# Kernel optimization log

Hardware: AMD Instinct MI355X
Metric: run time of the kernel (lower is better)

The kernel has to match this reference:

```python
import jax, jax.numpy as jnp
import numpy as np

H = 2048          # hidden_size
NH = 16           # num_attention_heads
HD = H // NH      # head_dim = 128
RD = HD // 2      # rotary dim = 64
LAT = H // 8      # latent_dim = 256
B, S = 2, 2048
BASE = 10000.0


def rotary_emb(seq_len, dtype=jnp.float32):
    # DeepseekRotaryEmbedding(dim=RD): inv_freq over arange(0, RD, 2)
    inv_freq = 1.0 / (BASE ** (np.arange(0, RD, 2, dtype=np.float32) / RD))  # [RD//2]
    pos = jnp.arange(seq_len, dtype=dtype)
    sincos = pos[:, None] * jnp.asarray(inv_freq, dtype)                     # [S, RD//2]
    return jnp.concatenate([jnp.sin(sincos), jnp.cos(sincos)], axis=-1)      # [S, RD]


def apply_rope(x, emb):
    # x: [B, S, NH, RD]; emb: [S, RD] with sin first half, cos second half
    half = RD // 2
    x1, x2 = x[..., :half], x[..., half:]
    sin = emb[:, None, :half]   # [S, 1, half] broadcast over heads
    cos = emb[:, None, half:]
    return jnp.concatenate([x1 * cos - x2 * sin, x1 * sin + x2 * cos], axis=-1)


def setup_inputs() -> dict:
    key = jax.random.key(0)
    ks = jax.random.split(key, 9)
    def w(k, shape):
        return jax.random.normal(k, shape, dtype=jnp.float32) * (1.0 / np.sqrt(shape[-1]))
    return {
        "hidden_states": jax.random.normal(ks[0], (B, S, H), dtype=jnp.float32),
        "W_kv_d": w(ks[1], (LAT, H)),
        "W_q_d": w(ks[2], (LAT, H)),
        "W_k_u": w(ks[3], (H // 2, LAT)),
        "W_q_u": w(ks[4], (H // 2, LAT)),
        "W_v_u": w(ks[5], (H, LAT)),
        "W_rope_k": w(ks[6], (H // 2, H)),
        "W_rope_q": w(ks[7], (H // 2, LAT)),
        "W_o": w(ks[8], (H, H)),
    }


def reference(hidden_states, W_kv_d, W_q_d, W_k_u, W_q_u, W_v_u, W_rope_k, W_rope_q, W_o):
    x = hidden_states                                   # [B, S, H]
    kv_d = x @ W_kv_d.T                                 # [B, S, LAT]
    q_d = x @ W_q_d.T                                   # [B, S, LAT]
    k_c = (kv_d @ W_k_u.T).reshape(B, S, NH, RD)        # content half of k
    q_c = (q_d @ W_q_u.T).reshape(B, S, NH, RD)
    v = (kv_d @ W_v_u.T).reshape(B, S, NH, HD)
    k_r = (x @ W_rope_k.T).reshape(B, S, NH, RD)
    q_r = (q_d @ W_rope_q.T).reshape(B, S, NH, RD)

    emb = rotary_emb(S, x.dtype)                        # [S, RD]
    q_r = apply_rope(q_r, emb)
    k_r = apply_rope(k_r, emb)

    q = jnp.concatenate([q_c, q_r], axis=-1)            # [B, S, NH, HD]
    k = jnp.concatenate([k_c, k_r], axis=-1)

    scale = 1.0 / np.sqrt(HD)                           # SDPA default scale
    scores = jnp.einsum("bqhd,bkhd->bhqk", q, k) * scale
    causal = jnp.tril(jnp.ones((S, S), dtype=bool))
    scores = jnp.where(causal, scores, jnp.finfo(scores.dtype).min)
    probs = jax.nn.softmax(scores, axis=-1)
    y = jnp.einsum("bhqk,bkhd->bqhd", probs, v).reshape(B, S, H)
    return y @ W_o.T
```

## Files before the change

kernel.cpp:

```cpp
#include <hip/hip_runtime.h>

typedef unsigned short u16;
typedef unsigned int u32;
typedef __attribute__((ext_vector_type(8))) short bf16x8;
typedef __attribute__((ext_vector_type(4))) float f32x4;

#define DEVI static __device__ __forceinline__

DEVI u16 f2b(float f){
  u32 x = __float_as_uint(f);
  return (u16)((x + 0x7fffu + ((x >> 16) & 1u)) >> 16);
}
DEVI float b2f(u16 u){ return __uint_as_float(((u32)u) << 16); }
DEVI float2 up2(u32 u){
  return make_float2(__uint_as_float(u << 16), __uint_as_float(u & 0xffff0000u));
}
DEVI u32 pk2(float a, float b){
  u32 ua = __float_as_uint(a) + 0x8000u;
  u32 ub = __float_as_uint(b) + 0x8000u;
  return (ua >> 16) | (ub & 0xffff0000u);
}
DEVI void gload16(const u16* g, u16* l){
  __builtin_amdgcn_global_load_lds((const __attribute__((address_space(1))) void*)g,
                                   (__attribute__((address_space(3))) void*)l,
                                   16, 0, 0);
}

#define QSCALE 0.12751744900929456f

struct CSrc { const float* s[9]; };
__global__ void cvt_all(CSrc cs, u16* __restrict__ xb, u16* __restrict__ wcat){
  int i = blockIdx.x * 256 + threadIdx.x;
  if (i >= 4259840) return;
  const float4* s; int lo, di; uint2* d;
  if (i < 2097152){
    s = (const float4*)cs.s[0]; lo = 0; di = i; d = (uint2*)xb;
  } else {
    int j = i - 2097152; di = j; d = (uint2*)wcat;
    if      (j <  131072){ s = (const float4*)cs.s[1]; lo = 0;       }
    else if (j <  262144){ s = (const float4*)cs.s[2]; lo = 131072;  }
    else if (j <  786432){ s = (const float4*)cs.s[3]; lo = 262144;  }
    else if (j <  851968){ s = (const float4*)cs.s[4]; lo = 786432;  }
    else if (j <  917504){ s = (const float4*)cs.s[5]; lo = 851968;  }
    else if (j <  983040){ s = (const float4*)cs.s[6]; lo = 917504;  }
    else if (j < 1114112){ s = (const float4*)cs.s[7]; lo = 983040;  }
    else                 { s = (const float4*)cs.s[8]; lo = 1114112; }
  }
  float4 f = s[di - lo];
  u32 a = (u32)f2b(f.x) | ((u32)f2b(f.y) << 16);
  u32 b = (u32)f2b(f.z) | ((u32)f2b(f.w) << 16);
  d[di] = make_uint2(a, b);
}

template<int MODE>
__global__ __launch_bounds__(256, 2)
void gemm_bt(const u16* __restrict__ A, int lda, const u16* __restrict__ W,
             void* __restrict__ D, int N, int K){
  __shared__ u16 As[128 * 64];
  __shared__ u16 Bs[128 * 64];
  const int tid = threadIdx.x;
  const int wave = tid >> 6, lane = tid & 63;
  const int lr = lane & 15, lk = lane >> 4;
  int bid = blockIdx.y * gridDim.x + blockIdx.x;
  const int nwg = gridDim.x * gridDim.y;
  bid = (bid & 7) * (nwg >> 3) + (bid >> 3);
  const int bx = bid % gridDim.x, by = bid / gridDim.x;
  const int m0 = by * 128, n0 = bx * 128;
  const int wm = wave >> 1, wn = wave & 1;
  f32x4 acc[4][4] = {};

  const int srow = tid >> 3;
  const int scol = ((tid & 7) ^ (srow & 7)) << 3;
  const u16* ag = A + (size_t)(m0 + srow) * lda + scol;
  const u16* bg = W + (size_t)(n0 + srow) * K + scol;
  u16* lA = As + wave * 512;
  u16* lB = Bs + wave * 512;

  for (int k0 = 0; k0 < K; k0 += 64){
    __syncthreads();
    #pragma unroll
    for (int s = 0; s < 4; ++s){
      gload16(ag + (size_t)s * 32 * lda + k0, lA + s * 2048);
      gload16(bg + (size_t)s * 32 * K   + k0, lB + s * 2048);
    }
    asm volatile("s_waitcnt vmcnt(0)" ::: "memory");
    __syncthreads();
    #pragma unroll
    for (int ks = 0; ks < 2; ++ks){
      bf16x8 af[4], bfr[4];
      const int perm = ((ks * 4 + lk) ^ (lr & 7)) << 3;
      #pragma unroll
      for (int i = 0; i < 4; i++)
        af[i] = *(const bf16x8*)(As + (wm * 64 + i * 16 + lr) * 64 + perm);
      #pragma unroll
      for (int j = 0; j < 4; j++)
        bfr[j] = *(const bf16x8*)(Bs + (wn * 64 + j * 16 + lr) * 64 + perm);
      #pragma unroll
      for (int i = 0; i < 4; i++)
        #pragma unroll
        for (int j = 0; j < 4; j++)
          acc[i][j] = __builtin_amdgcn_mfma_f32_16x16x32_bf16(af[i], bfr[j], acc[i][j], 0, 0, 0);
    }
  }

  const int rb = (lane >> 4) * 4, cl = lane & 15;
  #pragma unroll
  for (int i = 0; i < 4; i++){
    #pragma unroll
    for (int j = 0; j < 4; j++){
      const int mb = m0 + wm * 64 + i * 16 + rb;
      const int n  = n0 + wn * 64 + j * 16 + cl;
      #pragma unroll
      for (int r = 0; r < 4; r++){
        int m = mb + r;
        float v = acc[i][j][r];
        if (MODE == 0) ((u16*)D)[(size_t)m * N + n] = f2b(v);
        else           ((float*)D)[(size_t)m * N + n] = v;
      }
    }
  }
}

__global__ __launch_bounds__(256, 2)
void gemm_up(const u16* __restrict__ dcat, const u16* __restrict__ qW,
             const u16* __restrict__ kvW, u16* __restrict__ qbuf,
             u16* __restrict__ qrp, u16* __restrict__ kbuf, u16* __restrict__ vt){
  __shared__ u16 As[128 * 32];
  __shared__ u16 Bs[128 * 32];
  const int tid = threadIdx.x;
  const int wave = tid >> 6, lane = tid & 63;
  const int lr = lane & 15, lk = lane >> 4;
  int bid = blockIdx.y * 40 + blockIdx.x;
  bid = (bid & 7) * 160 + (bid >> 3);
  const int bx = bid % 40, by = bid / 40;
  const bool qside = bx < 16;
  const u16* A = qside ? dcat + 256 : dcat;
  const u16* W = qside ? qW : kvW;
  const int n0 = (qside ? bx : bx - 16) * 128;
  const int m0 = by * 128;
  const int wm = wave >> 1, wn = wave & 1;
  f32x4 acc[4][4] = {};

  const u16* a0 = A + (size_t)(m0 + (tid >> 2)) * 1536 + (tid & 3) * 8;
  const u16* a1 = a0 + (size_t)64 * 1536;
  const u16* b0 = W + (size_t)(n0 + (tid >> 2)) * 256 + (tid & 3) * 8;
  const u16* b1 = b0 + (size_t)64 * 256;
  u16* lA0 = As + wave * 512;  u16* lA1 = As + 2048 + wave * 512;
  u16* lB0 = Bs + wave * 512;  u16* lB1 = Bs + 2048 + wave * 512;

  for (int k0 = 0; k0 < 256; k0 += 32){
    __syncthreads();
    gload16(a0 + k0, lA0);
    gload16(a1 + k0, lA1);
    gload16(b0 + k0, lB0);
    gload16(b1 + k0, lB1);
    asm volatile("s_waitcnt vmcnt(0)" ::: "memory");
    __syncthreads();
    bf16x8 af[4], bfr[4];
    #pragma unroll
    for (int i = 0; i < 4; i++)
      af[i] = *(const bf16x8*)(As + (wm * 64 + i * 16 + lr) * 32 + lk * 8);
    #pragma unroll
    for (int j = 0; j < 4; j++)
      bfr[j] = *(const bf16x8*)(Bs + (wn * 64 + j * 16 + lr) * 32 + lk * 8);
    #pragma unroll
    for (int i = 0; i < 4; i++)
      #pragma unroll
      for (int j = 0; j < 4; j++)
        acc[i][j] = __builtin_amdgcn_mfma_f32_16x16x32_bf16(af[i], bfr[j], acc[i][j], 0, 0, 0);
  }

  const int rb = (lane >> 4) * 4, cl = lane & 15;
  #pragma unroll
  for (int i = 0; i < 4; i++){
    #pragma unroll
    for (int j = 0; j < 4; j++){
      const int mb = m0 + wm * 64 + i * 16 + rb;
      const int n  = n0 + wn * 64 + j * 16 + cl;
      if (!qside && n >= 1024){
        int n1 = n - 1024, h = n1 >> 7, d = n1 & 127, b = mb >> 11, s = mb & 2047;
        u32 lo = (u32)f2b(acc[i][j][0]) | ((u32)f2b(acc[i][j][1]) << 16);
        u32 hi = (u32)f2b(acc[i][j][2]) | ((u32)f2b(acc[i][j][3]) << 16);
        *(uint2*)(vt + (((size_t)(b * 16 + h) * 128 + d) * 2048 + s)) = make_uint2(lo, hi);
      } else {
        #pragma unroll
        for (int r = 0; r < 4; r++){
          int m = mb + r;
          float v = acc[i][j][r];
          if (qside){
            if (n < 1024){
              qrp[(size_t)m * 1024 + n] = f2b(v);
            } else {
              int n1 = n - 1024, h = n1 >> 6, d = n1 & 63;
              qbuf[(((size_t)(m >> 11) * 16 + h) * 2048 + (m & 2047)) * 128 + d] = f2b(v * QSCALE);
            }
          } else {
            int h = n >> 6, d = n & 63;
            kbuf[(((size_t)(m >> 11) * 16 + h) * 2048 + (m & 2047)) * 128 + d] = f2b(v);
          }
        }
      }
    }
  }
}

__global__ void rope_k(const u16* __restrict__ qrp, const u16* __restrict__ dcat,
                       u16* __restrict__ Qb, u16* __restrict__ Kb){
  int idx = blockIdx.x * 256 + threadIdx.x;
  if (idx >= (1 << 21)) return;
  int j = idx & 31, h = (idx >> 5) & 15, s = (idx >> 9) & 2047, b = (idx >> 20) & 1;
  float inv = exp2f((float)j * (-13.287712379549449f / 32.0f));
  float ang = (float)s * inv;
  float sn = sinf(ang), cs = cosf(ang);
  size_t soq = ((size_t)(b * 2048 + s)) * 1024 + h * 64 + j;
  size_t sok = ((size_t)(b * 2048 + s)) * 1536 + 512 + h * 64 + j;
  size_t dd = (((size_t)(b * 16 + h)) * 2048 + s) * 128;
  {
    float x1 = b2f(qrp[soq]), x2 = b2f(qrp[soq + 32]);
    Qb[dd + 64 + j] = f2b((x1 * cs - x2 * sn) * QSCALE);
    Qb[dd + 96 + j] = f2b((x1 * sn + x2 * cs) * QSCALE);
  }
  {
    float x1 = b2f(dcat[sok]), x2 = b2f(dcat[sok + 32]);
    Kb[dd + 64 + j] = f2b(x1 * cs - x2 * sn);
    Kb[dd + 96 + j] = f2b(x1 * sn + x2 * cs);
  }
}

__global__ __launch_bounds__(512, 1)
void flash_part(const u16* __restrict__ Q, const u16* __restrict__ K,
                const u16* __restrict__ VT, u16* __restrict__ Op0,
                u16* __restrict__ Op1, float2* __restrict__ ML){
  __shared__ u16 k_s[3][8192];
  __shared__ u16 v_s[3][8192];
  __shared__ u16 p_s[8][2048];
  const int tid = threadIdx.x;
  const int w = tid >> 6, l = tid & 63;
  const int lr = l & 15, hk = l >> 4;
  const int bh = blockIdx.x;
  const int qt = 7 - blockIdx.y;
  const int z  = blockIdx.z;
  const int b = bh >> 4, h = bh & 15;
  const size_t base = (size_t)bh * 2048 * 128;
  const u16* Qb = Q + base;
  const u16* Kb = K + base;
  const u16* Vb = VT + base;
  u16* myp = p_s[w];
  const int q0 = qt * 256 + w * 32;
  const int T  = 2 * qt + 2;
  const int t0 = z * T;

  bf16x8 qa[2][4];
  #pragma unroll
  for (int mi = 0; mi < 2; mi++)
    #pragma unroll
    for (int ks = 0; ks < 4; ks++)
      qa[mi][ks] = *(const bf16x8*)(Qb + (size_t)(q0 + mi * 16 + lr) * 128 + ks * 32 + hk * 8);

  f32x4 o[2][8] = {};
  float mbase[2] = {-1e30f, -1e30f};
  float lsum[2] = {0.f, 0.f};

  auto STAGE_K = [&](int kt, int buf){
    #pragma unroll
    for (int it = 0; it < 2; ++it){
      int row = it * 32 + w * 4 + (l >> 4);
      gload16(Kb + (size_t)(kt * 64 + row) * 128 + (((l & 15) ^ (row & 15)) << 3),
              &k_s[buf][it * 4096 + w * 512]);
    }
  };
  auto STAGE_V = [&](int kt, int buf){
    #pragma unroll
    for (int it = 0; it < 2; ++it){
      int d = it * 64 + w * 8 + (l >> 3);
      gload16(Vb + (size_t)d * 2048 + kt * 64 + (((l & 7) ^ (d & 7)) << 3),
              &v_s[buf][it * 4096 + w * 512]);
    }
  };

  STAGE_V(t0, 0);
  STAGE_K(t0, 0);
  STAGE_K(t0 + 1, 1);
  asm volatile("s_waitcnt vmcnt(2)" ::: "memory");
  __builtin_amdgcn_s_barrier();

  for (int tt = 0; tt < T; ++tt){
    const int t = t0 + tt;
    const bool preV = (tt + 1 < T);
    const bool preK = (tt + 2 < T);
    if (preV) STAGE_V(t + 1, (tt + 1) % 3);
    if (preK) STAGE_K(t + 2, (tt + 2) % 3);

    const bool act = (t * 64 <= q0 + 31);
    if (act){
      const u16* ks_ = k_s[tt % 3];
      f32x4 sc[2][4] = {};
      #pragma unroll
      for (int ksd = 0; ksd < 4; ++ksd){
        bf16x8 kb[4];
        #pragma unroll
        for (int nj = 0; nj < 4; ++nj){
          int row = nj * 16 + lr;
          kb[nj] = *(const bf16x8*)(ks_ + row * 128 + (((ksd * 4 + hk) ^ lr) << 3));
        }
        __builtin_amdgcn_s_setprio(1);
        #pragma unroll
        for (int mi = 0; mi < 2; ++mi)
          #pragma unroll
          for (int nj = 0; nj < 4; ++nj)
            sc[mi][nj] = __builtin_amdgcn_mfma_f32_16x16x32_bf16(kb[nj], qa[mi][ksd], sc[mi][nj], 0, 0, 0);
        __builtin_amdgcn_s_setprio(0);
      }
      float lmax[2] = {-3e38f, -3e38f};
      if (t * 64 + 63 > q0){
        #pragma unroll
        for (int mi = 0; mi < 2; ++mi){
          int qrow = q0 + mi * 16 + lr;
          #pragma unroll
          for (int nj = 0; nj < 4; ++nj)
            #pragma unroll
            for (int r = 0; r < 4; ++r){
              int kc = t * 64 + nj * 16 + hk * 4 + r;
              float s = (kc <= qrow) ? sc[mi][nj][r] : -1e30f;
              sc[mi][nj][r] = s;
              lmax[mi] = fmaxf(lmax[mi], s);
            }
        }
      } else {
        #pragma unroll
        for (int mi = 0; mi < 2; ++mi)
          #pragma unroll
          for (int nj = 0; nj < 4; ++nj)
            #pragma unroll
            for (int r = 0; r < 4; ++r)
              lmax[mi] = fmaxf(lmax[mi], sc[mi][nj][r]);
      }
      if (__any((lmax[0] > mbase[0] + 8.f) || (lmax[1] > mbase[1] + 8.f))){
        #pragma unroll
        for (int mi = 0; mi < 2; ++mi){
          float mx = lmax[mi];
          mx = fmaxf(mx, __shfl_xor(mx, 16));
          mx = fmaxf(mx, __shfl_xor(mx, 32));
          float mnew = fmaxf(mbase[mi], mx);
          float alpha = exp2f(mbase[mi] - mnew);
          mbase[mi] = mnew;
          lsum[mi] *= alpha;
          #pragma unroll
          for (int dj = 0; dj < 8; ++dj)
            #pragma unroll
            for (int r = 0; r < 4; ++r) o[mi][dj][r] *= alpha;
        }
      }
      #pragma unroll
      for (int mi = 0; mi < 2; ++mi){
        u16* prow = myp + (mi * 16 + lr) * 64;
        float rs = 0.f;
        #pragma unroll
        for (int nj = 0; nj < 4; ++nj){
          float p0 = exp2f(sc[mi][nj][0] - mbase[mi]);
          float p1 = exp2f(sc[mi][nj][1] - mbase[mi]);
          float p2 = exp2f(sc[mi][nj][2] - mbase[mi]);
          float p3 = exp2f(sc[mi][nj][3] - mbase[mi]);
          rs += (p0 + p1) + (p2 + p3);
          *(uint2*)(prow + ((nj * 16 + hk * 4) ^ ((lr & 7) << 3))) =
              make_uint2(pk2(p0, p1), pk2(p2, p3));
        }
        lsum[mi] += rs;
      }
    }

    if (preK)      asm volatile("s_waitcnt vmcnt(4)" ::: "memory");
    else if (preV) asm volatile("s_waitcnt vmcnt(2)" ::: "memory");
    else           asm volatile("s_waitcnt vmcnt(0)" ::: "memory");
    __builtin_amdgcn_s_barrier();
    asm volatile("s_waitcnt lgkmcnt(0)" ::: "memory");
    __builtin_amdgcn_sched_barrier(0);

    if (act){
      const u16* vs_ = v_s[tt % 3];
      #pragma unroll
      for (int kk = 0; kk < 2; ++kk){
        bf16x8 pb[2], va[8];
        #pragma unroll
        for (int mi = 0; mi < 2; ++mi)
          pb[mi] = *(const bf16x8*)(myp + (mi * 16 + lr) * 64 +
                     ((kk * 32 + hk * 8) ^ ((lr & 7) << 3)));
        #pragma unroll
        for (int dj = 0; dj < 8; ++dj){
          int d = dj * 16 + lr;
          va[dj] = *(const bf16x8*)(vs_ + d * 64 + (((kk * 4 + hk) ^ (lr & 7)) << 3));
        }
        __builtin_amdgcn_s_setprio(1);
        #pragma unroll
        for (int mi = 0; mi < 2; ++mi)
          #pragma unroll
          for (int dj = 0; dj < 8; ++dj)
            o[mi][dj] = __builtin_amdgcn_mfma_f32_16x16x32_bf16(va[dj], pb[mi], o[mi][dj], 0, 0, 0);
        __builtin_amdgcn_s_setprio(0);
      }
    }
  }

  u16* Op = z ? Op1 : Op0;
  u16* scr = myp;
  #pragma unroll
  for (int mi = 0; mi < 2; ++mi){
    float lt = lsum[mi];
    lt += __shfl_xor(lt, 16);
    lt += __shfl_xor(lt, 32);
    if (hk == 0){
      float2 v; v.x = mbase[mi]; v.y = lt;
      ML[((size_t)z * 32 + bh) * 2048 + qt * 256 + w * 32 + mi * 16 + lr] = v;
    }
    #pragma unroll
    for (int dj = 0; dj < 8; ++dj){
      u32 a = (u32)f2b(o[mi][dj][0]) | ((u32)f2b(o[mi][dj][1]) << 16);
      u32 c = (u32)f2b(o[mi][dj][2]) | ((u32)f2b(o[mi][dj][3]) << 16);
      *(uint2*)(scr + lr * 128 + ((dj * 16 + hk * 4) ^ ((lr & 7) << 3))) = make_uint2(a, c);
    }
    asm volatile("s_waitcnt lgkmcnt(0)" ::: "memory");
    __builtin_amdgcn_sched_barrier(0);
    #pragma unroll
    for (int rr = 0; rr < 4; ++rr){
      int row = rr * 4 + hk;
      uint4 vv = *(const uint4*)(scr + row * 128 + ((lr * 8) ^ ((row & 7) << 3)));
      *(uint4*)(Op + ((size_t)(b * 2048) + qt * 256 + w * 32 + mi * 16 + row) * 2048
                    + h * 128 + lr * 8) = vv;
    }
    asm volatile("s_waitcnt lgkmcnt(0)" ::: "memory");
    __builtin_amdgcn_sched_barrier(0);
  }
}

__global__ void merge_k(const u16* __restrict__ Op0, const u16* __restrict__ Op1,
                        const float2* __restrict__ ML, u16* __restrict__ Y){
  int i = blockIdx.x * 256 + threadIdx.x;
  if (i >= (1 << 20)) return;
  int row = i >> 8;
  int c8 = (i & 255) << 3;
  int b = row >> 11, s = row & 2047, h = c8 >> 7;
  int bh = b * 16 + h;
  float2 ml0 = ML[(size_t)bh * 2048 + s];
  float2 ml1 = ML[(size_t)(32 + bh) * 2048 + s];
  float m = fmaxf(ml0.x, ml1.x);
  float w0 = exp2f(ml0.x - m), w1 = exp2f(ml1.x - m);
  float inv = 1.0f / fmaxf(ml0.y * w0 + ml1.y * w1, 1e-30f);
  size_t off = (size_t)row * 2048 + c8;
  uint4 a = *(const uint4*)(Op0 + off);
  uint4 c = *(const uint4*)(Op1 + off);
  u32 res[4];
  u32 au[4] = {a.x, a.y, a.z, a.w};
  u32 cu[4] = {c.x, c.y, c.z, c.w};
  #pragma unroll
  for (int j = 0; j < 4; ++j){
    float2 f = up2(au[j]), g = up2(cu[j]);
    float r0 = (f.x * w0 + g.x * w1) * inv;
    float r1 = (f.y * w0 + g.y * w1) * inv;
    res[j] = (u32)f2b(r0) | ((u32)f2b(r1) << 16);
  }
  *(uint4*)(Y + off) = make_uint4(res[0], res[1], res[2], res[3]);
}

extern "C" void kernel_launch(void* const* d_in, const int* in_sizes, int n_in,
                              void* d_out, int out_size, void* d_ws, size_t ws_size,
                              hipStream_t stream){
  u16* p = (u16*)d_ws;
  auto alloc = [&](size_t n){ u16* r = p; p += n; return r; };
  u16* wcat = alloc(8650752);
  u16* downW  = wcat;
  u16* qcatW  = wcat + 3145728;
  u16* kvcatW = wcat + 3670016;
  u16* wo     = wcat + 4456448;
  u16* xb   = alloc(8388608);
  u16* dcat = alloc(6291456);
  u16* qrp  = alloc(4194304);
  u16* qbuf = alloc(8388608);
  u16* kbuf = alloc(8388608);
  u16* vt   = alloc(8388608);
  u16* ybuf = alloc(8388608);
  float2* ml = (float2*)alloc(524288);

  CSrc cs;
  cs.s[0] = (const float*)d_in[0];
  cs.s[1] = (const float*)d_in[1];
  cs.s[2] = (const float*)d_in[2];
  cs.s[3] = (const float*)d_in[6];
  cs.s[4] = (const float*)d_in[7];
  cs.s[5] = (const float*)d_in[4];
  cs.s[6] = (const float*)d_in[3];
  cs.s[7] = (const float*)d_in[5];
  cs.s[8] = (const float*)d_in[8];
  cvt_all<<<16640, 256, 0, stream>>>(cs, xb, wcat);

  dim3 blk(256);
  gemm_bt<0><<<dim3(12, 32), blk, 0, stream>>>(xb, 2048, downW, dcat, 1536, 2048);
  gemm_up<<<dim3(40, 32), blk, 0, stream>>>(dcat, qcatW, kvcatW, qbuf, qrp, kbuf, vt);
  rope_k<<<(1 << 21) / 256, 256, 0, stream>>>(qrp, dcat, qbuf, kbuf);
  u16* op0 = xb;
  u16* op1 = dcat;
  flash_part<<<dim3(32, 8, 2), dim3(512), 0, stream>>>(qbuf, kbuf, vt, op0, op1, ml);
  merge_k<<<4096, 256, 0, stream>>>(op0, op1, ml, ybuf);
  gemm_bt<3><<<dim3(16, 32), blk, 0, stream>>>(ybuf, 2048, wo, d_out, 2048, 2048);
}
```

Measured before the change: 196.7 us.

## Double-buffer LDS tiles in projection GEMMs to overlap loads with MFMA

Both projection GEMM kernels now use two LDS buffers and prefetch the next K tile with async global-to-LDS loads while computing on the current one. A partial vmcnt wait replaces the full drain. gemm_up also moves to a K-tile of 64 with the XOR-swizzled layout, halving its iteration count. LDS use doubles to 64KB per block, which may limit occupancy at two blocks per CU.

```diff
diff --git a/kernel.cpp b/kernel.cpp
--- a/kernel.cpp
+++ b/kernel.cpp
@@ -56,8 +56,8 @@
 __global__ __launch_bounds__(256, 2)
 void gemm_bt(const u16* __restrict__ A, int lda, const u16* __restrict__ W,
              void* __restrict__ D, int N, int K){
-  __shared__ u16 As[128 * 64];
-  __shared__ u16 Bs[128 * 64];
+  __shared__ u16 As[2][128 * 64];
+  __shared__ u16 Bs[2][128 * 64];
   const int tid = threadIdx.x;
   const int wave = tid >> 6, lane = tid & 63;
   const int lr = lane & 15, lk = lane >> 4;
@@ -67,40 +67,49 @@
   const int bx = bid % gridDim.x, by = bid / gridDim.x;
   const int m0 = by * 128, n0 = bx * 128;
   const int wm = wave >> 1, wn = wave & 1;
+  const int nt = K >> 6;
   f32x4 acc[4][4] = {};
 
   const int srow = tid >> 3;
   const int scol = ((tid & 7) ^ (srow & 7)) << 3;
   const u16* ag = A + (size_t)(m0 + srow) * lda + scol;
   const u16* bg = W + (size_t)(n0 + srow) * K + scol;
-  u16* lA = As + wave * 512;
-  u16* lB = Bs + wave * 512;
-
-  for (int k0 = 0; k0 < K; k0 += 64){
-    __syncthreads();
+
+  auto STAGE = [&](int t, int bf){
     #pragma unroll
     for (int s = 0; s < 4; ++s){
-      gload16(ag + (size_t)s * 32 * lda + k0, lA + s * 2048);
-      gload16(bg + (size_t)s * 32 * K   + k0, lB + s * 2048);
-    }
-    asm volatile("s_waitcnt vmcnt(0)" ::: "memory");
-    __syncthreads();
+      gload16(ag + (size_t)s * 32 * lda + t * 64, &As[bf][s * 2048 + wave * 512]);
+      gload16(bg + (size_t)s * 32 * K   + t * 64, &Bs[bf][s * 2048 + wave * 512]);
+    }
+  };
+
+  STAGE(0, 0);
+  for (int t = 0; t < nt; ++t){
+    const bool pre = (t + 1 < nt);
+    if (pre) STAGE(t + 1, (t + 1) & 1);
+    if (pre) asm volatile("s_waitcnt vmcnt(8)" ::: "memory");
+    else     asm volatile("s_waitcnt vmcnt(0)" ::: "memory");
+    __builtin_amdgcn_s_barrier();
+    __builtin_amdgcn_sched_barrier(0);
+    const u16* As_ = As[t & 1];
+    const u16* Bs_ = Bs[t & 1];
     #pragma unroll
     for (int ks = 0; ks < 2; ++ks){
       bf16x8 af[4], bfr[4];
       const int perm = ((ks * 4 + lk) ^ (lr & 7)) << 3;
       #pragma unroll
       for (int i = 0; i < 4; i++)
-        af[i] = *(const bf16x8*)(As + (wm * 64 + i * 16 + lr) * 64 + perm);
+        af[i] = *(const bf16x8*)(As_ + (wm * 64 + i * 16 + lr) * 64 + perm);
       #pragma unroll
       for (int j = 0; j < 4; j++)
-        bfr[j] = *(const bf16x8*)(Bs + (wn * 64 + j * 16 + lr) * 64 + perm);
+        bfr[j] = *(const bf16x8*)(Bs_ + (wn * 64 + j * 16 + lr) * 64 + perm);
       #pragma unroll
       for (int i = 0; i < 4; i++)
         #pragma unroll
         for (int j = 0; j < 4; j++)
           acc[i][j] = __builtin_amdgcn_mfma_f32_16x16x32_bf16(af[i], bfr[j], acc[i][j], 0, 0, 0);
     }
+    __builtin_amdgcn_s_barrier();
   }
 
   const int rb = (lane >> 4) * 4, cl = lane & 15;
@@ -125,8 +134,8 @@
 void gemm_up(const u16* __restrict__ dcat, const u16* __restrict__ qW,
              const u16* __restrict__ kvW, u16* __restrict__ qbuf,
              u16* __restrict__ qrp, u16* __restrict__ kbuf, u16* __restrict__ vt){
-  __shared__ u16 As[128 * 32];
-  __shared__ u16 Bs[128 * 32];
+  __shared__ u16 As[2][128 * 64];
+  __shared__ u16 Bs[2][128 * 64];
   const int tid = threadIdx.x;
   const int wave = tid >> 6, lane = tid & 63;
   const int lr = lane & 15, lk = lane >> 4;
@@ -141,33 +150,47 @@
   const int wm = wave >> 1, wn = wave & 1;
   f32x4 acc[4][4] = {};
 
-  const u16* a0 = A + (size_t)(m0 + (tid >> 2)) * 1536 + (tid & 3) * 8;
-  const u16* a1 = a0 + (size_t)64 * 1536;
-  const u16* b0 = W + (size_t)(n0 + (tid >> 2)) * 256 + (tid & 3) * 8;
-  const u16* b1 = b0 + (size_t)64 * 256;
-  u16* lA0 = As + wave * 512;  u16* lA1 = As + 2048 + wave * 512;
-  u16* lB0 = Bs + wave * 512;  u16* lB1 = Bs + 2048 + wave * 512;
-
-  for (int k0 = 0; k0 < 256; k0 += 32){
-    __syncthreads();
-    gload16(a0 + k0, lA0);
-    gload16(a1 + k0, lA1);
-    gload16(b0 + k0, lB0);
-    gload16(b1 + k0, lB1);
-    asm volatile("s_waitcnt vmcnt(0)" ::: "memory");
-    __syncthreads();
-    bf16x8 af[4], bfr[4];
-    #pragma unroll
-    for (int i = 0; i < 4; i++)
-      af[i] = *(const bf16x8*)(As + (wm * 64 + i * 16 + lr) * 32 + lk * 8);
-    #pragma unroll
-    for (int j = 0; j < 4; j++)
-      bfr[j] = *(const bf16x8*)(Bs + (wn * 64 + j * 16 + lr) * 32 + lk * 8);
-    #pragma unroll
-    for (int i = 0; i < 4; i++)
+  const int srow = tid >> 3;
+  const int scol = ((tid & 7) ^ (srow & 7)) << 3;
+  const u16* ag = A + (size_t)(m0 + srow) * 1536 + scol;
+  const u16* bg = W + (size_t)(n0 + srow) * 256 + scol;
+
+  auto STAGE = [&](int t, int bf){
+    #pragma unroll
+    for (int s = 0; s < 4; ++s){
+      gload16(ag + (size_t)s * 32 * 1536 + t * 64, &As[bf][s * 2048 + wave * 512]);
+      gload16(bg + (size_t)s * 32 * 256  + t * 64, &Bs[bf][s * 2048 + wave * 512]);
+    }
+  };
+
+  STAGE(0, 0);
+  #pragma unroll
+  for (int t = 0; t < 4; ++t){
+    const bool pre = (t + 1 < 4);
+    if (pre) STAGE(t + 1, (t + 1) & 1);
+    if (pre) asm volatile("s_waitcnt vmcnt(8)" ::: "memory");
+    else     asm volatile("s_waitcnt vmcnt(0)" ::: "memory");
+    __builtin_amdgcn_s_barrier();
+    __builtin_amdgcn_sched_barrier(0);
+    const u16* As_ = As[t & 1];
+    const u16* Bs_ = Bs[t & 1];
+    #pragma unroll
+    for (int ks = 0; ks < 2; ++ks){
+      bf16x8 af[4], bfr[4];
+      const int perm = ((ks * 4 + lk) ^ (lr & 7)) << 3;
+      #pragma unroll
+      for (int i = 0; i < 4; i++)
+        af[i] = *(const bf16x8*)(As_ + (wm * 64 + i * 16 + lr) * 64 + perm);
       #pragma unroll
       for (int j = 0; j < 4; j++)
-        acc[i][j] = __builtin_amdgcn_mfma_f32_16x16x32_bf16(af[i], bfr[j], acc[i][j], 0, 0, 0);
+        bfr[j] = *(const bf16x8*)(Bs_ + (wn * 64 + j * 16 + lr) * 64 + perm);
+      #pragma unroll
+      for (int i = 0; i < 4; i++)
+        #pragma unroll
+        for (int j = 0; j < 4; j++)
+          acc[i][j] = __builtin_amdgcn_mfma_f32_16x16x32_bf16(af[i], bfr[j], acc[i][j], 0, 0, 0);
+    }
+    __builtin_amdgcn_s_barrier();
   }
 
   const int rb = (lane >> 4) * 4, cl = lane & 15;
```

After: 202.1 us. 2.7% more time.
